# Optimization experiments

Hardware: AMD Instinct MI355X
Metric: run time of the kernel (lower is better)

Reference implementation:

```python
import jax, jax.numpy as jnp
import numpy as np

NEG_SLOPE = 0.2
N_NODES = 50000
N_EDGES = 800000


def _gat_layer(x, src, dst, W, a_src, a_dst, b):
    """PyG GATConv (concat=True, dropout=0) with self-loops already in (src, dst)."""
    N = x.shape[0]
    H, C = a_src.shape
    h = (x @ W).reshape(N, H, C)                       # [N, H, C]
    alpha_s = jnp.sum(h * a_src, axis=-1)              # [N, H]
    alpha_d = jnp.sum(h * a_dst, axis=-1)              # [N, H]
    e = jax.nn.leaky_relu(alpha_s[src] + alpha_d[dst], NEG_SLOPE)  # [E, H]
    # numerically stable segment softmax over incoming edges of each dst node
    emax = jax.ops.segment_max(e, dst, num_segments=N)
    p = jnp.exp(e - emax[dst])
    denom = jax.ops.segment_sum(p, dst, num_segments=N)
    alpha = p / denom[dst]                             # [E, H]
    msg = h[src] * alpha[:, :, None]                   # [E, H, C]
    out = jax.ops.segment_sum(msg, dst, num_segments=N)
    return out.reshape(N, H * C) + b


def setup_inputs() -> dict:
    key = jax.random.key(0)
    ks = jax.random.split(key, 16)
    x = jax.random.normal(ks[0], (N_NODES, 128), dtype=jnp.float32)
    edge_index = jax.random.randint(ks[1], (2, N_EDGES), 0, N_NODES, dtype=jnp.int64)

    def glorot(k, shape, fan_in):
        return jax.random.normal(k, shape, dtype=jnp.float32) * (1.0 / np.sqrt(fan_in))

    # layer 0: in=128, heads=4, out=32
    W0 = glorot(ks[2], (128, 4 * 32), 128)
    as0 = glorot(ks[3], (4, 32), 32)
    ad0 = glorot(ks[4], (4, 32), 32)
    b0 = jnp.zeros((128,), dtype=jnp.float32)
    # layer 1: in=128, heads=4, out=32
    W1 = glorot(ks[5], (128, 4 * 32), 128)
    as1 = glorot(ks[6], (4, 32), 32)
    ad1 = glorot(ks[7], (4, 32), 32)
    b1 = jnp.zeros((128,), dtype=jnp.float32)
    # layer 2: in=128, heads=1, out=128
    W2 = glorot(ks[8], (128, 1 * 128), 128)
    as2 = glorot(ks[9], (1, 128), 128)
    ad2 = glorot(ks[10], (1, 128), 128)
    b2 = jnp.zeros((128,), dtype=jnp.float32)
    return {"x": x, "edge_index": edge_index,
            "W0": W0, "as0": as0, "ad0": ad0, "b0": b0,
            "W1": W1, "as1": as1, "ad1": ad1, "b1": b1,
            "W2": W2, "as2": as2, "ad2": ad2, "b2": b2}


def reference(x, edge_index, W0, as0, ad0, b0, W1, as1, ad1, b1, W2, as2, ad2, b2):
    N = x.shape[0]
    loops = jnp.arange(N, dtype=edge_index.dtype)
    src = jnp.concatenate([edge_index[0], loops])  # GATConv add_self_loops=True
    dst = jnp.concatenate([edge_index[1], loops])
    for (W, a_s, a_d, b) in ((W0, as0, ad0, b0), (W1, as1, ad1, b1), (W2, as2, ad2, b2)):
        x = jax.nn.relu(_gat_layer(x, src, dst, W, a_s, a_d, b))
    return x
```

## Files before the change

kernel.cpp:

```cpp
#include <hip/hip_runtime.h>

#define NEG_SLOPE 0.2f
#define CAP 64

using f32x4 = __attribute__((ext_vector_type(4))) float;
using bf16x8 = __attribute__((ext_vector_type(8))) short;

__device__ inline unsigned short bf16_rne(float f) {
    unsigned int u = __float_as_uint(f);
    return (unsigned short)((u + 0x7FFF + ((u >> 16) & 1)) >> 16);
}
__device__ inline float bf16_tof(unsigned short h) {
    return __uint_as_float(((unsigned int)h) << 16);
}

__global__ void zero_kernel(int* __restrict__ p, int n) {
    int i = blockIdx.x * blockDim.x + threadIdx.x;
    if (i < n) p[i] = 0;
}

__global__ void build_kernel(const void* __restrict__ ei_raw, int E,
                             int* __restrict__ cnt, int* __restrict__ bucket,
                             int* __restrict__ ovf_src,
                             int* __restrict__ ovf_dst,
                             int* __restrict__ ovf_cnt) {
    const int* as32 = (const int*)ei_raw;
    const long long* as64 = (const long long*)ei_raw;
    bool is64 = true;
    for (int i = 0; i < 16; ++i) {
        long long v = as64[i];
        if (!(v >= 0 && v < 2147483648LL)) { is64 = false; }
    }
    int i = blockIdx.x * blockDim.x + threadIdx.x;
    if (i < E) {
        int s, d;
        if (is64) {
            s = (int)as64[i];
            d = (int)as64[(size_t)E + i];
        } else {
            s = as32[i];
            d = as32[(size_t)E + i];
        }
        int p = atomicAdd(&cnt[d], 1);
        if (p < CAP) {
            bucket[(size_t)d * CAP + p] = s;
        } else {
            int q = atomicAdd(ovf_cnt, 1);
            ovf_src[q] = s;
            ovf_dst[q] = d;
        }
    }
}

__global__ void wprep_kernel(const float* __restrict__ W0,
                             const float* __restrict__ W1,
                             const float* __restrict__ W2,
                             unsigned short* __restrict__ wf) {
    int tid = blockIdx.x * blockDim.x + threadIdx.x;
    if (tid >= 3 * 2048) return;
    int layer = tid >> 11;
    int rem = tid & 2047;
    int kstep = rem >> 9;
    int ct = (rem >> 6) & 7;
    int lane = rem & 63;
    const float* W = (layer == 0) ? W0 : (layer == 1) ? W1 : W2;
    unsigned short* hi = wf + (size_t)layer * 32768 +
                         ((size_t)(kstep * 8 + ct) * 64 + lane) * 8;
    unsigned short* lo = hi + 16384;
#pragma unroll
    for (int j = 0; j < 8; ++j) {
        int k = kstep * 32 + (lane >> 4) * 8 + j;
        int n = ct * 16 + (lane & 15);
        float f = W[k * 128 + n];
        unsigned short h = bf16_rne(f);
        hi[j] = h;
        lo[j] = bf16_rne(f - bf16_tof(h));
    }
}

template <int H>
__global__ __launch_bounds__(256) void gemm_mfma_kernel(
    const float* __restrict__ X, const unsigned short* __restrict__ wf_hi,
    const unsigned short* __restrict__ wf_lo, const float* __restrict__ asrc,
    const float* __restrict__ adst, float* __restrict__ Hout,
    float* __restrict__ alpha_s, float* __restrict__ alpha_d, int N) {
    int t = threadIdx.x;
    int wv = t >> 6;
    int l = t & 63;
    int m = l & 15;
    int quad = l >> 4;
    int row0 = blockIdx.x * 64 + wv * 16;

    f32x4 acc[8];
#pragma unroll
    for (int ct = 0; ct < 8; ++ct) acc[ct] = (f32x4){0.f, 0.f, 0.f, 0.f};

    int arow = row0 + m;
    bool okA = arow < N;
    const float4* X4 = (const float4*)X;

    for (int kstep = 0; kstep < 4; ++kstep) {
        float4 a0 = make_float4(0.f, 0.f, 0.f, 0.f);
        float4 a1 = make_float4(0.f, 0.f, 0.f, 0.f);
        if (okA) {
            a0 = X4[(size_t)arow * 32 + kstep * 8 + quad * 2];
            a1 = X4[(size_t)arow * 32 + kstep * 8 + quad * 2 + 1];
        }
        float av8[8] = {a0.x, a0.y, a0.z, a0.w, a1.x, a1.y, a1.z, a1.w};
        bf16x8 ah, al;
#pragma unroll
        for (int j = 0; j < 8; ++j) {
            unsigned short h = bf16_rne(av8[j]);
            ah[j] = (short)h;
            al[j] = (short)bf16_rne(av8[j] - bf16_tof(h));
        }
#pragma unroll
        for (int ct = 0; ct < 8; ++ct) {
            size_t boff = ((size_t)(kstep * 8 + ct) * 64 + l) * 8;
            bf16x8 bh = *(const bf16x8*)(wf_hi + boff);
            bf16x8 bl = *(const bf16x8*)(wf_lo + boff);
            acc[ct] = __builtin_amdgcn_mfma_f32_16x16x32_bf16(ah, bh, acc[ct], 0, 0, 0);
            acc[ct] = __builtin_amdgcn_mfma_f32_16x16x32_bf16(al, bh, acc[ct], 0, 0, 0);
            acc[ct] = __builtin_amdgcn_mfma_f32_16x16x32_bf16(ah, bl, acc[ct], 0, 0, 0);
        }
    }

#pragma unroll
    for (int reg = 0; reg < 4; ++reg) {
        int row = row0 + quad * 4 + reg;
        if (row < N) {
#pragma unroll
            for (int ct = 0; ct < 8; ++ct)
                Hout[(size_t)row * 128 + ct * 16 + m] = acc[ct][reg];
        }
    }

    float av[8], dv[8];
#pragma unroll
    for (int ct = 0; ct < 8; ++ct) {
        av[ct] = asrc[ct * 16 + m];
        dv[ct] = adst[ct * 16 + m];
    }
#pragma unroll
    for (int reg = 0; reg < 4; ++reg) {
        int row = row0 + quad * 4 + reg;
        if (H == 4) {
            float ps[4], pd[4];
#pragma unroll
            for (int hh = 0; hh < 4; ++hh) {
                ps[hh] = acc[2 * hh][reg] * av[2 * hh] +
                         acc[2 * hh + 1][reg] * av[2 * hh + 1];
                pd[hh] = acc[2 * hh][reg] * dv[2 * hh] +
                         acc[2 * hh + 1][reg] * dv[2 * hh + 1];
            }
#pragma unroll
            for (int o = 1; o < 16; o <<= 1) {
#pragma unroll
                for (int hh = 0; hh < 4; ++hh) {
                    ps[hh] += __shfl_xor(ps[hh], o);
                    pd[hh] += __shfl_xor(pd[hh], o);
                }
            }
            if (m == 0 && row < N) {
#pragma unroll
                for (int hh = 0; hh < 4; ++hh) {
                    alpha_s[(size_t)row * 4 + hh] = ps[hh];
                    alpha_d[(size_t)row * 4 + hh] = pd[hh];
                }
            }
        } else {
            float ps = 0.f, pd = 0.f;
#pragma unroll
            for (int ct = 0; ct < 8; ++ct) {
                ps += acc[ct][reg] * av[ct];
                pd += acc[ct][reg] * dv[ct];
            }
#pragma unroll
            for (int o = 1; o < 16; o <<= 1) {
                ps += __shfl_xor(ps, o);
                pd += __shfl_xor(pd, o);
            }
            if (m == 0 && row < N) {
                alpha_s[row] = ps;
                alpha_d[row] = pd;
            }
        }
    }
}

template <int H>
__global__ __launch_bounds__(128) void gather_kernel(
    const float* __restrict__ h, const float* __restrict__ as_,
    const float* __restrict__ ad_, const int* __restrict__ cnt,
    const int* __restrict__ bucket, const int* __restrict__ ovf_src,
    const int* __restrict__ ovf_dst, const int* __restrict__ ovf_cnt,
    const float* __restrict__ bias, float* __restrict__ out, int N) {
    __shared__ int s_src[4][32];
    __shared__ float s_w[4][32 * H];
    int t = threadIdx.x;
    int wv = t >> 6;
    int lane = t & 63;
    int hw = lane >> 5;
    int l = lane & 31;
    int sub = wv * 2 + hw;
    int n = blockIdx.x * 4 + sub;
    if (n >= N) return;

    int deg = cnt[n];
    int total = deg + 1;
    int totalb = min(deg, CAP) + 1;
    int onum = (deg > CAP) ? *ovf_cnt : 0;
    const int* bk = bucket + (size_t)n * CAP;

    float adv[H];
#pragma unroll
    for (int hh = 0; hh < H; ++hh) adv[hh] = ad_[(size_t)n * H + hh];

    float sv[H];
    float m[H];
#pragma unroll
    for (int hh = 0; hh < H; ++hh) m[hh] = -3.4e38f;
    int total0 = min(total, 32);
    if (l < total0) {
        int src = (l == 0) ? n : bk[l - 1];
        s_src[sub][l] = src;
        if (H == 4) {
            float4 a4 = ((const float4*)as_)[src];
            sv[0] = a4.x + adv[0];
            sv[1] = a4.y + adv[1];
            sv[2] = a4.z + adv[2];
            sv[3] = a4.w + adv[3];
        } else {
            sv[0] = as_[src] + adv[0];
        }
#pragma unroll
        for (int hh = 0; hh < H; ++hh) {
            float s = sv[hh];
            s = (s > 0.f) ? s : NEG_SLOPE * s;
            sv[hh] = s;
            m[hh] = s;
        }
    }
    for (int idx = l + 32; idx < totalb; idx += 32) {
        int src = bk[idx - 1];
#pragma unroll
        for (int hh = 0; hh < H; ++hh) {
            float s = as_[(size_t)src * H + hh] + adv[hh];
            s = (s > 0.f) ? s : NEG_SLOPE * s;
            m[hh] = fmaxf(m[hh], s);
        }
    }
    for (int e = 0; e < onum; ++e) {
        if (ovf_dst[e] == n && l == 0) {
            int src = ovf_src[e];
#pragma unroll
            for (int hh = 0; hh < H; ++hh) {
                float s = as_[(size_t)src * H + hh] + adv[hh];
                s = (s > 0.f) ? s : NEG_SLOPE * s;
                m[hh] = fmaxf(m[hh], s);
            }
        }
    }
#pragma unroll
    for (int o = 16; o > 0; o >>= 1)
#pragma unroll
        for (int hh = 0; hh < H; ++hh) m[hh] = fmaxf(m[hh], __shfl_xor(m[hh], o));

    float p[H];
    float dsum[H];
#pragma unroll
    for (int hh = 0; hh < H; ++hh) dsum[hh] = 0.f;
    if (l < total0) {
#pragma unroll
        for (int hh = 0; hh < H; ++hh) {
            p[hh] = __expf(sv[hh] - m[hh]);
            dsum[hh] = p[hh];
        }
    }
    for (int idx = l + 32; idx < totalb; idx += 32) {
        int src = bk[idx - 1];
#pragma unroll
        for (int hh = 0; hh < H; ++hh) {
            float s = as_[(size_t)src * H + hh] + adv[hh];
            s = (s > 0.f) ? s : NEG_SLOPE * s;
            dsum[hh] += __expf(s - m[hh]);
        }
    }
    for (int e = 0; e < onum; ++e) {
        if (ovf_dst[e] == n && l == 0) {
            int src = ovf_src[e];
#pragma unroll
            for (int hh = 0; hh < H; ++hh) {
                float s = as_[(size_t)src * H + hh] + adv[hh];
                s = (s > 0.f) ? s : NEG_SLOPE * s;
                dsum[hh] += __expf(s - m[hh]);
            }
        }
    }
#pragma unroll
    for (int o = 16; o > 0; o >>= 1)
#pragma unroll
        for (int hh = 0; hh < H; ++hh) dsum[hh] += __shfl_xor(dsum[hh], o);
    float inv[H];
#pragma unroll
    for (int hh = 0; hh < H; ++hh) inv[hh] = 1.f / dsum[hh];

    if (l < total0) {
#pragma unroll
        for (int hh = 0; hh < H; ++hh) s_w[sub][l * H + hh] = p[hh] * inv[hh];
    }

    const int head_t = (H == 1) ? 0 : (l >> 3);
    float4 acc = make_float4(0.f, 0.f, 0.f, 0.f);
    const float4* __restrict__ h4 = (const float4*)h;
    for (int base = 0; base < totalb; base += 32) {
        int cnt2 = min(32, totalb - base);
        if (base > 0 && l < cnt2) {
            int src = bk[base + l - 1];
            s_src[sub][l] = src;
#pragma unroll
            for (int hh = 0; hh < H; ++hh) {
                float s = as_[(size_t)src * H + hh] + adv[hh];
                s = (s > 0.f) ? s : NEG_SLOPE * s;
                s_w[sub][l * H + hh] = __expf(s - m[hh]) * inv[hh];
            }
        }
        __builtin_amdgcn_wave_barrier();
        int j = 0;
        for (; j + 8 <= cnt2; j += 8) {
            int ts[8];
            float ws[8];
            float4 vs[8];
#pragma unroll
            for (int u = 0; u < 8; ++u) {
                ts[u] = s_src[sub][j + u];
                ws[u] = s_w[sub][(j + u) * H + head_t];
            }
#pragma unroll
            for (int u = 0; u < 8; ++u) vs[u] = h4[(size_t)ts[u] * 32 + l];
#pragma unroll
            for (int u = 0; u < 8; ++u) {
                acc.x += ws[u] * vs[u].x;
                acc.y += ws[u] * vs[u].y;
                acc.z += ws[u] * vs[u].z;
                acc.w += ws[u] * vs[u].w;
            }
        }
        for (; j + 4 <= cnt2; j += 4) {
            int ts[4];
            float ws[4];
            float4 vs[4];
#pragma unroll
            for (int u = 0; u < 4; ++u) {
                ts[u] = s_src[sub][j + u];
                ws[u] = s_w[sub][(j + u) * H + head_t];
            }
#pragma unroll
            for (int u = 0; u < 4; ++u) vs[u] = h4[(size_t)ts[u] * 32 + l];
#pragma unroll
            for (int u = 0; u < 4; ++u) {
                acc.x += ws[u] * vs[u].x;
                acc.y += ws[u] * vs[u].y;
                acc.z += ws[u] * vs[u].z;
                acc.w += ws[u] * vs[u].w;
            }
        }
        for (; j < cnt2; ++j) {
            int sj = s_src[sub][j];
            float wj = s_w[sub][j * H + head_t];
            float4 hv = h4[(size_t)sj * 32 + l];
            acc.x += wj * hv.x; acc.y += wj * hv.y;
            acc.z += wj * hv.z; acc.w += wj * hv.w;
        }
        __builtin_amdgcn_wave_barrier();
    }
    for (int e = 0; e < onum; ++e) {
        if (ovf_dst[e] == n) {
            int src = ovf_src[e];
            int hh = head_t;
            float s = as_[(size_t)src * H + hh] + adv[hh];
            s = (s > 0.f) ? s : NEG_SLOPE * s;
            float wj = __expf(s - m[hh]) * inv[hh];
            float4 hv = h4[(size_t)src * 32 + l];
            acc.x += wj * hv.x; acc.y += wj * hv.y;
            acc.z += wj * hv.z; acc.w += wj * hv.w;
        }
    }
    float4 bv = ((const float4*)bias)[l];
    float4 o4;
    o4.x = fmaxf(acc.x + bv.x, 0.f);
    o4.y = fmaxf(acc.y + bv.y, 0.f);
    o4.z = fmaxf(acc.z + bv.z, 0.f);
    o4.w = fmaxf(acc.w + bv.w, 0.f);
    ((float4*)out)[(size_t)n * 32 + l] = o4;
}

extern "C" void kernel_launch(void* const* d_in, const int* in_sizes, int n_in,
                              void* d_out, int out_size, void* d_ws,
                              size_t ws_size, hipStream_t stream) {
    const float* x   = (const float*)d_in[0];
    const void*  ei  = d_in[1];
    const float* W0  = (const float*)d_in[2];
    const float* as0 = (const float*)d_in[3];
    const float* ad0 = (const float*)d_in[4];
    const float* b0  = (const float*)d_in[5];
    const float* W1  = (const float*)d_in[6];
    const float* as1 = (const float*)d_in[7];
    const float* ad1 = (const float*)d_in[8];
    const float* b1  = (const float*)d_in[9];
    const float* W2  = (const float*)d_in[10];
    const float* as2 = (const float*)d_in[11];
    const float* ad2 = (const float*)d_in[12];
    const float* b2  = (const float*)d_in[13];

    int N = in_sizes[0] / 128;
    int E = in_sizes[1] / 2;
    float* out = (float*)d_out;

    float* h       = (float*)d_ws;
    float* alpha_s = h + (size_t)N * 128;
    float* alpha_d = alpha_s + (size_t)N * 4;
    int*   cnt     = (int*)(alpha_d + (size_t)N * 4);
    int*   ovf_c   = cnt + N;
    int*   bucket  = ovf_c + 1;
    int*   ovf_src = bucket + (size_t)N * CAP;
    int*   ovf_dst = ovf_src + E;
    unsigned short* wf = (unsigned short*)(ovf_dst + E);

    int eb = (E + 255) / 256;
    int nb = (N + 1 + 255) / 256;

    zero_kernel<<<nb, 256, 0, stream>>>(cnt, N + 1);
    wprep_kernel<<<24, 256, 0, stream>>>(W0, W1, W2, wf);
    build_kernel<<<eb, 256, 0, stream>>>(ei, E, cnt, bucket, ovf_src, ovf_dst, ovf_c);

    int gb = (N + 63) / 64;
    int wb = (N + 3) / 4;

    gemm_mfma_kernel<4><<<gb, 256, 0, stream>>>(x, wf, wf + 16384, as0, ad0,
                                                h, alpha_s, alpha_d, N);
    gather_kernel<4><<<wb, 128, 0, stream>>>(h, alpha_s, alpha_d, cnt, bucket,
                                             ovf_src, ovf_dst, ovf_c, b0, out, N);

    gemm_mfma_kernel<4><<<gb, 256, 0, stream>>>(out, wf + 32768, wf + 49152,
                                                as1, ad1, h, alpha_s, alpha_d, N);
    gather_kernel<4><<<wb, 128, 0, stream>>>(h, alpha_s, alpha_d, cnt, bucket,
                                             ovf_src, ovf_dst, ovf_c, b1, out, N);

    gemm_mfma_kernel<1><<<gb, 256, 0, stream>>>(out, wf + 65536, wf + 81920,
                                                as2, ad2, h, alpha_s, alpha_d, N);
    gather_kernel<1><<<wb, 128, 0, stream>>>(h, alpha_s, alpha_d, cnt, bucket,
                                             ovf_src, ovf_dst, ovf_c, b2, out, N);
}
```

Before: 408.9 us.

## Store GAT node features as bf16 for gathers and fuse setup kernels

Layers 0 and 1 now write the projected node features h in bf16 and the gather kernels read 8-byte packed values instead of 16-byte float4, halving the random-gather traffic. The weight-prep and counter-zeroing kernels are merged into one launch, and the edge-bucket build is folded into the first GEMM launch as extra blocks, removing launches and serialization. The 4-wide unroll tail in the gather is dropped. Accuracy drops slightly because features are rounded to bf16 before aggregation.

```diff
diff --git a/kernel.cpp b/kernel.cpp
--- a/kernel.cpp
+++ b/kernel.cpp
@@ -14,24 +14,51 @@
     return __uint_as_float(((unsigned int)h) << 16);
 }
 
-__global__ void zero_kernel(int* __restrict__ p, int n) {
-    int i = blockIdx.x * blockDim.x + threadIdx.x;
-    if (i < n) p[i] = 0;
-}
-
-__global__ void build_kernel(const void* __restrict__ ei_raw, int E,
-                             int* __restrict__ cnt, int* __restrict__ bucket,
-                             int* __restrict__ ovf_src,
-                             int* __restrict__ ovf_dst,
-                             int* __restrict__ ovf_cnt) {
+__global__ void prep_kernel(const float* __restrict__ W0,
+                            const float* __restrict__ W1,
+                            const float* __restrict__ W2,
+                            unsigned short* __restrict__ wf,
+                            int* __restrict__ cnt, int nz) {
+    if (blockIdx.x < 24) {
+        int tid = blockIdx.x * 256 + threadIdx.x;
+        if (tid >= 3 * 2048) return;
+        int layer = tid >> 11;
+        int rem = tid & 2047;
+        int kstep = rem >> 9;
+        int ct = (rem >> 6) & 7;
+        int lane = rem & 63;
+        const float* W = (layer == 0) ? W0 : (layer == 1) ? W1 : W2;
+        unsigned short* hi = wf + (size_t)layer * 32768 +
+                             ((size_t)(kstep * 8 + ct) * 64 + lane) * 8;
+        unsigned short* lo = hi + 16384;
+#pragma unroll
+        for (int j = 0; j < 8; ++j) {
+            int k = kstep * 32 + (lane >> 4) * 8 + j;
+            int n = ct * 16 + (lane & 15);
+            float f = W[k * 128 + n];
+            unsigned short h = bf16_rne(f);
+            hi[j] = h;
+            lo[j] = bf16_rne(f - bf16_tof(h));
+        }
+    } else {
+        int i = (blockIdx.x - 24) * 256 + threadIdx.x;
+        if (i < nz) cnt[i] = 0;
+    }
+}
+
+__device__ inline void build_body(int i, const void* __restrict__ ei_raw,
+                                  int E, int* __restrict__ cnt,
+                                  int* __restrict__ bucket,
+                                  int* __restrict__ ovf_src,
+                                  int* __restrict__ ovf_dst,
+                                  int* __restrict__ ovf_cnt) {
     const int* as32 = (const int*)ei_raw;
     const long long* as64 = (const long long*)ei_raw;
     bool is64 = true;
-    for (int i = 0; i < 16; ++i) {
-        long long v = as64[i];
+    for (int k = 0; k < 16; ++k) {
+        long long v = as64[k];
         if (!(v >= 0 && v < 2147483648LL)) { is64 = false; }
     }
-    int i = blockIdx.x * blockDim.x + threadIdx.x;
     if (i < E) {
         int s, d;
         if (is64) {
@@ -52,44 +79,21 @@
     }
 }
 
-__global__ void wprep_kernel(const float* __restrict__ W0,
-                             const float* __restrict__ W1,
-                             const float* __restrict__ W2,
-                             unsigned short* __restrict__ wf) {
-    int tid = blockIdx.x * blockDim.x + threadIdx.x;
-    if (tid >= 3 * 2048) return;
-    int layer = tid >> 11;
-    int rem = tid & 2047;
-    int kstep = rem >> 9;
-    int ct = (rem >> 6) & 7;
-    int lane = rem & 63;
-    const float* W = (layer == 0) ? W0 : (layer == 1) ? W1 : W2;
-    unsigned short* hi = wf + (size_t)layer * 32768 +
-                         ((size_t)(kstep * 8 + ct) * 64 + lane) * 8;
-    unsigned short* lo = hi + 16384;
-#pragma unroll
-    for (int j = 0; j < 8; ++j) {
-        int k = kstep * 32 + (lane >> 4) * 8 + j;
-        int n = ct * 16 + (lane & 15);
-        float f = W[k * 128 + n];
-        unsigned short h = bf16_rne(f);
-        hi[j] = h;
-        lo[j] = bf16_rne(f - bf16_tof(h));
-    }
-}
-
-template <int H>
-__global__ __launch_bounds__(256) void gemm_mfma_kernel(
-    const float* __restrict__ X, const unsigned short* __restrict__ wf_hi,
-    const unsigned short* __restrict__ wf_lo, const float* __restrict__ asrc,
-    const float* __restrict__ adst, float* __restrict__ Hout,
-    float* __restrict__ alpha_s, float* __restrict__ alpha_d, int N) {
+template <int H, bool BF16OUT>
+__device__ inline void gemm_body(int bid, const float* __restrict__ X,
+                                 const unsigned short* __restrict__ wf_hi,
+                                 const unsigned short* __restrict__ wf_lo,
+                                 const float* __restrict__ asrc,
+                                 const float* __restrict__ adst,
+                                 void* __restrict__ Hout,
+                                 float* __restrict__ alpha_s,
+                                 float* __restrict__ alpha_d, int N) {
     int t = threadIdx.x;
     int wv = t >> 6;
     int l = t & 63;
     int m = l & 15;
     int quad = l >> 4;
-    int row0 = blockIdx.x * 64 + wv * 16;
+    int row0 = bid * 64 + wv * 16;
 
     f32x4 acc[8];
 #pragma unroll
@@ -129,9 +133,17 @@
     for (int reg = 0; reg < 4; ++reg) {
         int row = row0 + quad * 4 + reg;
         if (row < N) {
-#pragma unroll
-            for (int ct = 0; ct < 8; ++ct)
-                Hout[(size_t)row * 128 + ct * 16 + m] = acc[ct][reg];
+            if (BF16OUT) {
+                unsigned short* hb = (unsigned short*)Hout;
+#pragma unroll
+                for (int ct = 0; ct < 8; ++ct)
+                    hb[(size_t)row * 128 + ct * 16 + m] = bf16_rne(acc[ct][reg]);
+            } else {
+                float* hf = (float*)Hout;
+#pragma unroll
+                for (int ct = 0; ct < 8; ++ct)
+                    hf[(size_t)row * 128 + ct * 16 + m] = acc[ct][reg];
+            }
         }
     }
 
@@ -188,9 +200,37 @@
     }
 }
 
-template <int H>
+template <int H, bool BF16OUT>
+__global__ __launch_bounds__(256) void gemm_build_kernel(
+    const float* __restrict__ X, const unsigned short* __restrict__ wf_hi,
+    const unsigned short* __restrict__ wf_lo, const float* __restrict__ asrc,
+    const float* __restrict__ adst, void* __restrict__ Hout,
+    float* __restrict__ alpha_s, float* __restrict__ alpha_d, int N, int gb,
+    const void* __restrict__ ei_raw, int E, int* __restrict__ cnt,
+    int* __restrict__ bucket, int* __restrict__ ovf_src,
+    int* __restrict__ ovf_dst, int* __restrict__ ovf_cnt) {
+    if ((int)blockIdx.x < gb) {
+        gemm_body<H, BF16OUT>(blockIdx.x, X, wf_hi, wf_lo, asrc, adst, Hout,
+                              alpha_s, alpha_d, N);
+    } else {
+        int i = ((int)blockIdx.x - gb) * 256 + threadIdx.x;
+        build_body(i, ei_raw, E, cnt, bucket, ovf_src, ovf_dst, ovf_cnt);
+    }
+}
+
+template <int H, bool BF16OUT>
+__global__ __launch_bounds__(256) void gemm_kernel(
+    const float* __restrict__ X, const unsigned short* __restrict__ wf_hi,
+    const unsigned short* __restrict__ wf_lo, const float* __restrict__ asrc,
+    const float* __restrict__ adst, void* __restrict__ Hout,
+    float* __restrict__ alpha_s, float* __restrict__ alpha_d, int N) {
+    gemm_body<H, BF16OUT>(blockIdx.x, X, wf_hi, wf_lo, asrc, adst, Hout,
+                          alpha_s, alpha_d, N);
+}
+
+template <int H, bool BF16IN>
 __global__ __launch_bounds__(128) void gather_kernel(
-    const float* __restrict__ h, const float* __restrict__ as_,
+    const void* __restrict__ hvp, const float* __restrict__ as_,
     const float* __restrict__ ad_, const int* __restrict__ cnt,
     const int* __restrict__ bucket, const int* __restrict__ ovf_src,
     const int* __restrict__ ovf_dst, const int* __restrict__ ovf_cnt,
@@ -312,7 +352,8 @@
 
     const int head_t = (H == 1) ? 0 : (l >> 3);
     float4 acc = make_float4(0.f, 0.f, 0.f, 0.f);
-    const float4* __restrict__ h4 = (const float4*)h;
+    const float4* __restrict__ h4 = (const float4*)hvp;
+    const uint2* __restrict__ hb2 = (const uint2*)hvp;
     for (int base = 0; base < totalb; base += 32) {
         int cnt2 = min(32, totalb - base);
         if (base > 0 && l < cnt2) {
@@ -330,47 +371,49 @@
         for (; j + 8 <= cnt2; j += 8) {
             int ts[8];
             float ws[8];
-            float4 vs[8];
 #pragma unroll
             for (int u = 0; u < 8; ++u) {
                 ts[u] = s_src[sub][j + u];
                 ws[u] = s_w[sub][(j + u) * H + head_t];
             }
-#pragma unroll
-            for (int u = 0; u < 8; ++u) vs[u] = h4[(size_t)ts[u] * 32 + l];
-#pragma unroll
-            for (int u = 0; u < 8; ++u) {
-                acc.x += ws[u] * vs[u].x;
-                acc.y += ws[u] * vs[u].y;
-                acc.z += ws[u] * vs[u].z;
-                acc.w += ws[u] * vs[u].w;
-            }
-        }
-        for (; j + 4 <= cnt2; j += 4) {
-            int ts[4];
-            float ws[4];
-            float4 vs[4];
-#pragma unroll
-            for (int u = 0; u < 4; ++u) {
-                ts[u] = s_src[sub][j + u];
-                ws[u] = s_w[sub][(j + u) * H + head_t];
-            }
-#pragma unroll
-            for (int u = 0; u < 4; ++u) vs[u] = h4[(size_t)ts[u] * 32 + l];
-#pragma unroll
-            for (int u = 0; u < 4; ++u) {
-                acc.x += ws[u] * vs[u].x;
-                acc.y += ws[u] * vs[u].y;
-                acc.z += ws[u] * vs[u].z;
-                acc.w += ws[u] * vs[u].w;
+            if (BF16IN) {
+                uint2 rv[8];
+#pragma unroll
+                for (int u = 0; u < 8; ++u) rv[u] = hb2[(size_t)ts[u] * 32 + l];
+#pragma unroll
+                for (int u = 0; u < 8; ++u) {
+                    acc.x += ws[u] * __uint_as_float(rv[u].x << 16);
+                    acc.y += ws[u] * __uint_as_float(rv[u].x & 0xFFFF0000u);
+                    acc.z += ws[u] * __uint_as_float(rv[u].y << 16);
+                    acc.w += ws[u] * __uint_as_float(rv[u].y & 0xFFFF0000u);
+                }
+            } else {
+                float4 vs[8];
+#pragma unroll
+                for (int u = 0; u < 8; ++u) vs[u] = h4[(size_t)ts[u] * 32 + l];
+#pragma unroll
+                for (int u = 0; u < 8; ++u) {
+                    acc.x += ws[u] * vs[u].x;
+                    acc.y += ws[u] * vs[u].y;
+                    acc.z += ws[u] * vs[u].z;
+                    acc.w += ws[u] * vs[u].w;
+                }
             }
         }
         for (; j < cnt2; ++j) {
             int sj = s_src[sub][j];
             float wj = s_w[sub][j * H + head_t];
-            float4 hv = h4[(size_t)sj * 32 + l];
-            acc.x += wj * hv.x; acc.y += wj * hv.y;
-            acc.z += wj * hv.z; acc.w += wj * hv.w;
+            if (BF16IN) {
+                uint2 rv = hb2[(size_t)sj * 32 + l];
+                acc.x += wj * __uint_as_float(rv.x << 16);
+                acc.y += wj * __uint_as_float(rv.x & 0xFFFF0000u);
+                acc.z += wj * __uint_as_float(rv.y << 16);
+                acc.w += wj * __uint_as_float(rv.y & 0xFFFF0000u);
+            } else {
+                float4 hv = h4[(size_t)sj * 32 + l];
+                acc.x += wj * hv.x; acc.y += wj * hv.y;
+                acc.z += wj * hv.z; acc.w += wj * hv.w;
+            }
         }
         __builtin_amdgcn_wave_barrier();
     }
@@ -381,9 +424,17 @@
             float s = as_[(size_t)src * H + hh] + adv[hh];
             s = (s > 0.f) ? s : NEG_SLOPE * s;
             float wj = __expf(s - m[hh]) * inv[hh];
-            float4 hv = h4[(size_t)src * 32 + l];
-            acc.x += wj * hv.x; acc.y += wj * hv.y;
-            acc.z += wj * hv.z; acc.w += wj * hv.w;
+            if (BF16IN) {
+                uint2 rv = hb2[(size_t)src * 32 + l];
+                acc.x += wj * __uint_as_float(rv.x << 16);
+                acc.y += wj * __uint_as_float(rv.x & 0xFFFF0000u);
+                acc.z += wj * __uint_as_float(rv.y << 16);
+                acc.w += wj * __uint_as_float(rv.y & 0xFFFF0000u);
+            } else {
+                float4 hv = h4[(size_t)src * 32 + l];
+                acc.x += wj * hv.x; acc.y += wj * hv.y;
+                acc.z += wj * hv.z; acc.w += wj * hv.w;
+            }
         }
     }
     float4 bv = ((const float4*)bias)[l];
@@ -429,26 +480,27 @@
 
     int eb = (E + 255) / 256;
     int nb = (N + 1 + 255) / 256;
-
-    zero_kernel<<<nb, 256, 0, stream>>>(cnt, N + 1);
-    wprep_kernel<<<24, 256, 0, stream>>>(W0, W1, W2, wf);
-    build_kernel<<<eb, 256, 0, stream>>>(ei, E, cnt, bucket, ovf_src, ovf_dst, ovf_c);
-
     int gb = (N + 63) / 64;
     int wb = (N + 3) / 4;
 
-    gemm_mfma_kernel<4><<<gb, 256, 0, stream>>>(x, wf, wf + 16384, as0, ad0,
-                                                h, alpha_s, alpha_d, N);
-    gather_kernel<4><<<wb, 128, 0, stream>>>(h, alpha_s, alpha_d, cnt, bucket,
-                                             ovf_src, ovf_dst, ovf_c, b0, out, N);
-
-    gemm_mfma_kernel<4><<<gb, 256, 0, stream>>>(out, wf + 32768, wf + 49152,
-                                                as1, ad1, h, alpha_s, alpha_d, N);
-    gather_kernel<4><<<wb, 128, 0, stream>>>(h, alpha_s, alpha_d, cnt, bucket,
-                                             ovf_src, ovf_dst, ovf_c, b1, out, N);
-
-    gemm_mfma_kernel<1><<<gb, 256, 0, stream>>>(out, wf + 65536, wf + 81920,
-                                                as2, ad2, h, alpha_s, alpha_d, N);
-    gather_kernel<1><<<wb, 128, 0, stream>>>(h, alpha_s, alpha_d, cnt, bucket,
-                                             ovf_src, ovf_dst, ovf_c, b2, out, N);
-}
+    prep_kernel<<<24 + nb, 256, 0, stream>>>(W0, W1, W2, wf, cnt, N + 1);
+
+    gemm_build_kernel<4, true><<<gb + eb, 256, 0, stream>>>(
+        x, wf, wf + 16384, as0, ad0, h, alpha_s, alpha_d, N, gb,
+        ei, E, cnt, bucket, ovf_src, ovf_dst, ovf_c);
+    gather_kernel<4, true><<<wb, 128, 0, stream>>>(h, alpha_s, alpha_d, cnt,
+                                                   bucket, ovf_src, ovf_dst,
+                                                   ovf_c, b0, out, N);
+
+    gemm_kernel<4, true><<<gb, 256, 0, stream>>>(out, wf + 32768, wf + 49152,
+                                                 as1, ad1, h, alpha_s, alpha_d, N);
+    gather_kernel<4, true><<<wb, 128, 0, stream>>>(h, alpha_s, alpha_d, cnt,
+                                                   bucket, ovf_src, ovf_dst,
+                                                   ovf_c, b1, out, N);
+
+    gemm_kernel<1, false><<<gb, 256, 0, stream>>>(out, wf + 65536, wf + 81920,
+                                                  as2, ad2, h, alpha_s, alpha_d, N);
+    gather_kernel<1, false><<<wb, 128, 0, stream>>>(h, alpha_s, alpha_d, cnt,
+                                                    bucket, ovf_src, ovf_dst,
+                                                    ovf_c, b2, out, N);
+}
```

After: 362.2 us. -11.4%, faster.
